# Kernel optimization log

Measured on AMD Instinct MI355X. Metric: run time of the kernel, lower is better.

Reference implementation:

```python
import jax, jax.numpy as jnp
import numpy as np

ALPHA = 5.0   # ATan surrogate sharpness
THETA = 1.0   # firing threshold
EPS = 1e-5    # BatchNorm eps

@jax.custom_vjp
def spike(x):
    # forward: heaviside; backward: ATan surrogate
    return (x >= 0.0).astype(x.dtype)

def _spike_fwd(x):
    return spike(x), x

def _spike_bwd(x, g):
    return (g * (ALPHA / 2.0) / (1.0 + (jnp.pi / 2.0 * ALPHA * x) ** 2),)

spike.defvjp(_spike_fwd, _spike_bwd)

def lif_layer(x, W, beta_p, gamma, bias, U0):
    # x: [B,T,J], W: [I,J] -> h: [B,T,I]
    h = jnp.einsum('btj,ij->bti', x, W)
    # BatchNorm1d in training mode: per-channel stats over B*T (biased var)
    mu = h.mean(axis=(0, 1))
    var = h.var(axis=(0, 1))
    h = (h - mu) * jax.lax.rsqrt(var + EPS) * gamma + bias
    beta = jax.nn.sigmoid(beta_p)  # [I]
    S0 = jnp.zeros_like(U0)

    def step(carry, xt):
        Ut, St = carry
        Ut = beta * (Ut - THETA * St) + (1.0 - beta) * xt  # soft reset
        St = spike(Ut - THETA)
        return (Ut, St), St

    _, o = jax.lax.scan(step, (U0, S0), jnp.swapaxes(h, 0, 1))  # [T,B,I]
    return jnp.swapaxes(o, 0, 1)  # [B,T,I]

def setup_inputs() -> dict:
    key = jax.random.key(0)
    B, T, J, H = 32, 1024, 1024, 2048
    ks = jax.random.split(key, 16)
    f32 = jnp.float32
    inp = {
        'x': jax.random.normal(ks[0], (B, T, J), f32),
        'W1': jax.random.normal(ks[1], (H, J), f32) / np.sqrt(J),
        'beta1': jax.random.uniform(ks[2], (H,), f32, 0.0, 4.0),
        'gamma1': jnp.ones((H,), f32),
        'bias1': jnp.zeros((H,), f32),
        'U01': jax.random.uniform(ks[3], (B, H), f32),
        'W2': jax.random.normal(ks[4], (H, H), f32) / np.sqrt(H),
        'beta2': jax.random.uniform(ks[5], (H,), f32, 0.0, 4.0),
        'gamma2': jnp.ones((H,), f32),
        'bias2': jnp.zeros((H,), f32),
        'U02': jax.random.uniform(ks[6], (B, H), f32),
        'W3': jax.random.normal(ks[7], (J, H), f32) / np.sqrt(H),
        'beta3': jax.random.uniform(ks[8], (J,), f32, 0.0, 4.0),
        'gamma3': jnp.ones((J,), f32),
        'bias3': jnp.zeros((J,), f32),
        'U03': jax.random.uniform(ks[9], (B, J), f32),
    }
    return inp

def reference(x, W1, beta1, gamma1, bias1, U01,
              W2, beta2, gamma2, bias2, U02,
              W3, beta3, gamma3, bias3, U03):
    h = lif_layer(x, W1, beta1, gamma1, bias1, U01)
    h = lif_layer(h, W2, beta2, gamma2, bias2, U02)
    h = lif_layer(h, W3, beta3, gamma3, bias3, U03)
    return h
```

## Files before the change

kernel.cpp:

```cpp
#include <hip/hip_runtime.h>
#include <hip/hip_bf16.h>
#include <cmath>

#define BB 32
#define TT 1024
#define JJ 1024
#define HH 2048
#define MM (BB * TT)
#define MHALF (MM / 2)

typedef short s8v __attribute__((ext_vector_type(8)));
typedef float f4v __attribute__((ext_vector_type(4)));
typedef unsigned int u4v __attribute__((ext_vector_type(4)));
union ABu { u4v u; s8v v; };

__device__ inline void split_bf16x3(float w, unsigned short& h,
                                    unsigned short& m, unsigned short& l) {
    __hip_bfloat16 bh = __float2bfloat16(w);
    const float fh = __bfloat162float(bh);
    const float r1 = w - fh;
    __hip_bfloat16 bm = __float2bfloat16(r1);
    const float fm = __bfloat162float(bm);
    __hip_bfloat16 bl = __float2bfloat16(r1 - fm);
    h = *(unsigned short*)&bh; m = *(unsigned short*)&bm; l = *(unsigned short*)&bl;
}

__global__ void split_w(const float* __restrict__ W,
                        unsigned short* __restrict__ ph,
                        unsigned short* __restrict__ pm,
                        unsigned short* __restrict__ pl, int n)
{
    const int i = blockIdx.x * 256 + threadIdx.x;
    if (i >= n) return;
    split_bf16x3(W[i], ph[i], pm[i], pl[i]);
}

__global__ __launch_bounds__(512) void mfma_spk_gemm(
    const unsigned char* __restrict__ S,
    const unsigned short* __restrict__ Wh,
    const unsigned short* __restrict__ Wm,
    const unsigned short* __restrict__ Wl,
    float* __restrict__ C, int M, int N, int K)
{
    __shared__ __align__(16) unsigned short Blds[2][3][2][128][32];
    const int tid = threadIdx.x;
    const int wv = tid >> 6;
    const int lane = tid & 63;
    const int wm = wv >> 1, wn = wv & 1;
    const int r16 = lane & 15, quad = lane >> 4;
    const int bm = blockIdx.x * 256;
    const int bn = blockIdx.y * 128;
    const int Kb = K >> 3;

    f4v acc[4][4] = {};

    const int rl = lane >> 2, chl = lane & 3;
    const int srow = wv * 16 + rl;
    const int kc = (chl - (srow >> 1)) & 3;
    const size_t soff = (size_t)(bn + srow) * K + kc * 8;
    const int ldsrow = wv * 16;

    size_t aoff[4];
#pragma unroll
    for (int ms = 0; ms < 4; ++ms)
        aoff[ms] = (size_t)(bm + wm * 64 + ms * 16 + r16) * Kb + quad;

    int bR[4], bC[4];
#pragma unroll
    for (int ns = 0; ns < 4; ++ns) {
        bR[ns] = wn * 64 + ns * 16 + r16;
        bC[ns] = ((quad + (bR[ns] >> 1)) & 3) * 8;
    }

    auto stage = [&](int buf, int p, int kh, int k0) {
        const unsigned short* Wp = (p == 0) ? Wh : (p == 1) ? Wm : Wl;
        __builtin_amdgcn_global_load_lds(
            (const __attribute__((address_space(1))) void*)(Wp + soff + k0 + kh * 32),
            (__attribute__((address_space(3))) void*)&Blds[buf][p][kh][ldsrow][0], 16, 0, 0);
    };

    unsigned int ab[2][4];
#pragma unroll
    for (int kh = 0; kh < 2; ++kh)
#pragma unroll
        for (int ms = 0; ms < 4; ++ms) ab[kh][ms] = S[aoff[ms] + kh * 4];

#pragma unroll
    for (int p = 0; p < 3; ++p)
#pragma unroll
        for (int kh = 0; kh < 2; ++kh) stage(0, p, kh, 0);

    const int NT = K >> 6;
    for (int t = 0; t < NT; ++t) {
        const int cur = t & 1, nxt = cur ^ 1;
        const int k0 = t << 6;
        __syncthreads();

        s8v afr[2][4];
#pragma unroll
        for (int kh = 0; kh < 2; ++kh)
#pragma unroll
            for (int ms = 0; ms < 4; ++ms) {
                ABu tu;
                const unsigned int b = ab[kh][ms];
                tu.u[0] = ((b        & 1u) * 0x3F80u) | (((b >> 1) & 1u) * 0x3F800000u);
                tu.u[1] = (((b >> 2) & 1u) * 0x3F80u) | (((b >> 3) & 1u) * 0x3F800000u);
                tu.u[2] = (((b >> 4) & 1u) * 0x3F80u) | (((b >> 5) & 1u) * 0x3F800000u);
                tu.u[3] = (((b >> 6) & 1u) * 0x3F80u) | (((b >> 7) & 1u) * 0x3F800000u);
                afr[kh][ms] = tu.v;
            }
        if (t + 1 < NT) {
            const size_t kb = (size_t)((k0 + 64) >> 3);
#pragma unroll
            for (int kh = 0; kh < 2; ++kh)
#pragma unroll
                for (int ms = 0; ms < 4; ++ms) ab[kh][ms] = S[aoff[ms] + kb + kh * 4];
        }

#pragma unroll
        for (int p = 0; p < 3; ++p)
#pragma unroll
            for (int kh = 0; kh < 2; ++kh) {
                s8v bf[4];
#pragma unroll
                for (int ns = 0; ns < 4; ++ns)
                    bf[ns] = *(const s8v*)&Blds[cur][p][kh][bR[ns]][bC[ns]];
                if (t + 1 < NT) stage(nxt, p, kh, k0 + 64);
                __builtin_amdgcn_s_setprio(1);
#pragma unroll
                for (int ms = 0; ms < 4; ++ms)
#pragma unroll
                    for (int ns = 0; ns < 4; ++ns)
                        acc[ms][ns] = __builtin_amdgcn_mfma_f32_16x16x32_bf16(
                            afr[kh][ms], bf[ns], acc[ms][ns], 0, 0, 0);
                __builtin_amdgcn_s_setprio(0);
            }
    }

#pragma unroll
    for (int ms = 0; ms < 4; ++ms)
#pragma unroll
        for (int ns = 0; ns < 4; ++ns) {
            const int row = bm + wm * 64 + ms * 16 + quad * 4;
            const int col = bn + wn * 64 + ns * 16 + r16;
#pragma unroll
            for (int r = 0; r < 4; ++r)
                C[(size_t)(row + r) * N + col] = acc[ms][ns][r];
        }
}

struct Sp3 { unsigned int o0, o1, o2; };

__device__ inline Sp3 split_pair(float x, float y)
{
    const unsigned int xb = __float_as_uint(x), yb = __float_as_uint(y);
    const unsigned int x0 = xb & 0xFFFF0000u,  y0 = yb & 0xFFFF0000u;
    const float xr1 = x - __uint_as_float(x0), yr1 = y - __uint_as_float(y0);
    const unsigned int x1b = __float_as_uint(xr1), y1b = __float_as_uint(yr1);
    const unsigned int x1 = x1b & 0xFFFF0000u, y1 = y1b & 0xFFFF0000u;
    const float xr2 = xr1 - __uint_as_float(x1), yr2 = yr1 - __uint_as_float(y1);
    Sp3 r;
    r.o0 = __builtin_amdgcn_perm(yb, xb, 0x07060302u);
    r.o1 = __builtin_amdgcn_perm(y1b, x1b, 0x07060302u);
    r.o2 = __builtin_amdgcn_perm(__float_as_uint(yr2), __float_as_uint(xr2), 0x07060302u);
    return r;
}

__global__ __launch_bounds__(256) void mfma_f32x3_gemm(
    const float* __restrict__ A,
    const unsigned short* __restrict__ Wh,
    const unsigned short* __restrict__ Wm,
    const unsigned short* __restrict__ Wl,
    float* __restrict__ C, int M, int N, int K)
{
    __shared__ __align__(16) unsigned short Blds[3][2][128][32];
    const int tid = threadIdx.x;
    const int wv = tid >> 6;
    const int lane = tid & 63;
    const int wm = wv >> 1, wn = wv & 1;
    const int r16 = lane & 15, quad = lane >> 4;

    const int lin = blockIdx.y * 16 + blockIdx.x;
    const int ppx = gridDim.y >> 3;
    const int xcd = lin & 7, li = lin >> 3;
    const int pm = xcd * ppx + (li >> 4);
    const int pn = li & 15;
    const int bm = pm * 128;
    const int bn = pn * 128;

    f4v acc[4][4] = {};

    const int rl = lane >> 2, chl = lane & 3;
    size_t soff[2];
    int ldsrow[2];
#pragma unroll
    for (int i = 0; i < 2; ++i) {
        const int r = wv * 32 + i * 16 + rl;
        const int kc = (chl - (r >> 1)) & 3;
        soff[i] = (size_t)(bn + r) * K + kc * 8;
        ldsrow[i] = wv * 32 + i * 16;
    }

    size_t aoff[4];
#pragma unroll
    for (int ms = 0; ms < 4; ++ms)
        aoff[ms] = (size_t)(bm + wm * 64 + ms * 16 + r16) * K + quad * 8;

    int bR[4], bC[4];
#pragma unroll
    for (int ns = 0; ns < 4; ++ns) {
        bR[ns] = wn * 64 + ns * 16 + r16;
        bC[ns] = ((quad + (bR[ns] >> 1)) & 3) * 8;
    }

    float4 av[2][4][2];
#pragma unroll
    for (int kh = 0; kh < 2; ++kh)
#pragma unroll
        for (int ms = 0; ms < 4; ++ms) {
            av[kh][ms][0] = *(const float4*)(A + aoff[ms] + kh * 32);
            av[kh][ms][1] = *(const float4*)(A + aoff[ms] + kh * 32 + 4);
        }

    for (int k0 = 0; k0 < K; k0 += 64) {
        __syncthreads();
#pragma unroll
        for (int i = 0; i < 2; ++i)
#pragma unroll
            for (int kh = 0; kh < 2; ++kh) {
                __builtin_amdgcn_global_load_lds(
                    (const __attribute__((address_space(1))) void*)(Wh + soff[i] + k0 + kh * 32),
                    (__attribute__((address_space(3))) void*)&Blds[0][kh][ldsrow[i]][0], 16, 0, 0);
                __builtin_amdgcn_global_load_lds(
                    (const __attribute__((address_space(1))) void*)(Wm + soff[i] + k0 + kh * 32),
                    (__attribute__((address_space(3))) void*)&Blds[1][kh][ldsrow[i]][0], 16, 0, 0);
                __builtin_amdgcn_global_load_lds(
                    (const __attribute__((address_space(1))) void*)(Wl + soff[i] + k0 + kh * 32),
                    (__attribute__((address_space(3))) void*)&Blds[2][kh][ldsrow[i]][0], 16, 0, 0);
            }
        s8v afr[3][2][4];
#pragma unroll
        for (int kh = 0; kh < 2; ++kh)
#pragma unroll
            for (int ms = 0; ms < 4; ++ms) {
                ABu t0, t1, t2;
                const float4 v0 = av[kh][ms][0];
                const float4 v1 = av[kh][ms][1];
                const Sp3 s0 = split_pair(v0.x, v0.y);
                const Sp3 s1 = split_pair(v0.z, v0.w);
                const Sp3 s2 = split_pair(v1.x, v1.y);
                const Sp3 s3 = split_pair(v1.z, v1.w);
                t0.u[0] = s0.o0; t1.u[0] = s0.o1; t2.u[0] = s0.o2;
                t0.u[1] = s1.o0; t1.u[1] = s1.o1; t2.u[1] = s1.o2;
                t0.u[2] = s2.o0; t1.u[2] = s2.o1; t2.u[2] = s2.o2;
                t0.u[3] = s3.o0; t1.u[3] = s3.o1; t2.u[3] = s3.o2;
                afr[0][kh][ms] = t0.v;
                afr[1][kh][ms] = t1.v;
                afr[2][kh][ms] = t2.v;
            }
        __syncthreads();
        if (k0 + 64 < K) {
#pragma unroll
            for (int kh = 0; kh < 2; ++kh)
#pragma unroll
                for (int ms = 0; ms < 4; ++ms) {
                    av[kh][ms][0] = *(const float4*)(A + aoff[ms] + k0 + 64 + kh * 32);
                    av[kh][ms][1] = *(const float4*)(A + aoff[ms] + k0 + 64 + kh * 32 + 4);
                }
        }
#pragma unroll
        for (int kh = 0; kh < 2; ++kh)
#pragma unroll
            for (int pw = 0; pw < 3; ++pw) {
                s8v bf[4];
#pragma unroll
                for (int ns = 0; ns < 4; ++ns)
                    bf[ns] = *(const s8v*)&Blds[pw][kh][bR[ns]][bC[ns]];
#pragma unroll
                for (int pa = 0; pa + pw < 3; ++pa)
#pragma unroll
                    for (int ms = 0; ms < 4; ++ms)
#pragma unroll
                        for (int ns = 0; ns < 4; ++ns)
                            acc[ms][ns] = __builtin_amdgcn_mfma_f32_16x16x32_bf16(
                                afr[pa][kh][ms], bf[ns], acc[ms][ns], 0, 0, 0);
            }
    }

#pragma unroll
    for (int ms = 0; ms < 4; ++ms)
#pragma unroll
        for (int ns = 0; ns < 4; ++ns) {
            const int row = bm + wm * 64 + ms * 16 + quad * 4;
            const int col = bn + wn * 64 + ns * 16 + r16;
#pragma unroll
            for (int r = 0; r < 4; ++r)
                C[(size_t)(row + r) * N + col] = acc[ms][ns][r];
        }
}

#define RCHUNK 128

__global__ void bn_stats_partial2(const float* __restrict__ hA,
                                  const float* __restrict__ hB,
                                  float* __restrict__ partial, int N)
{
    const int n = blockIdx.x * 256 + threadIdx.x;
    const int chunk = blockIdx.y;
    const int half = (MM / RCHUNK) / 2;
    const float* __restrict__ h = (chunk < half) ? hA : hB;
    const int cl = chunk & (half - 1);
    const float* p = h + (size_t)cl * RCHUNK * N + n;
    float s = 0.f, s2 = 0.f;
#pragma unroll 4
    for (int r = 0; r < RCHUNK; ++r) {
        const float v = p[(size_t)r * N];
        s += v;
        s2 = fmaf(v, v, s2);
    }
    partial[((size_t)chunk * 2 + 0) * N + n] = s;
    partial[((size_t)chunk * 2 + 1) * N + n] = s2;
}

__global__ void bn_stats_final(const float* __restrict__ partial,
                               float* __restrict__ stats,
                               int N, int nchunks)
{
    const int n = blockIdx.x * 256 + threadIdx.x;
    double s = 0.0, s2 = 0.0;
    for (int c = 0; c < nchunks; ++c) {
        s  += (double)partial[((size_t)c * 2 + 0) * N + n];
        s2 += (double)partial[((size_t)c * 2 + 1) * N + n];
    }
    const double inv_m = 1.0 / (double)MM;
    const double mu = s * inv_m;
    const double var = s2 * inv_m - mu * mu;
    stats[n]     = (float)mu;
    stats[N + n] = (float)(1.0 / sqrt(var + 1e-5));
}

#define LIF_STEP_PACK(hv)                                            \
    do {                                                             \
        const float hn = ((hv) - mu) * rstd * g + bi;                \
        u = beta * (u - s) + omb * hn;                               \
        const bool sp = (u - 1.0f) >= 0.f;                           \
        s = sp ? 1.f : 0.f;                                          \
        const unsigned long long mball = __ballot(sp);               \
        if (lead) bits[widx] = mball;                                \
        widx += nw;                                                  \
    } while (0)

#define LIF_LOAD8(buf, tbase)                                        \
    _Pragma("unroll")                                                \
    for (int j = 0; j < 8; ++j) {                                    \
        const int tl = (tbase) + j;                                  \
        buf[j] = h[base + (size_t)(tl < TT ? tl : TT - 1) * N];      \
    }

__global__ __launch_bounds__(64) void bn_lif_scan_pack2(
    const float* __restrict__ hA,
    const float* __restrict__ hB,
    unsigned long long* __restrict__ bits,
    const float* __restrict__ stats,
    const float* __restrict__ gamma,
    const float* __restrict__ bias,
    const float* __restrict__ beta_p,
    const float* __restrict__ U0,
    int N)
{
    const int n = blockIdx.x * 64 + threadIdx.x;
    const int b = blockIdx.y;
    const float* __restrict__ h = (b < BB / 2) ? hA : hB;
    const int bl = b & (BB / 2 - 1);
    const int nw = N >> 6;
    const float mu = stats[n];
    const float rstd = stats[N + n];
    const float g = gamma[n];
    const float bi = bias[n];
    const float beta = 1.f / (1.f + expf(-beta_p[n]));
    const float omb = 1.f - beta;
    float u = U0[(size_t)b * N + n];
    float s = 0.f;
    const size_t base = ((size_t)bl * TT) * N + n;
    size_t widx = ((size_t)b * TT) * nw + (n >> 6);
    const bool lead = (threadIdx.x & 63) == 0;

    float b0[8], b1[8], b2[8], b3[8];
    LIF_LOAD8(b0, 0);
    LIF_LOAD8(b1, 8);
    LIF_LOAD8(b2, 16);
    for (int t0 = 0; t0 < TT; t0 += 32) {
        LIF_LOAD8(b3, t0 + 24);
#pragma unroll
        for (int j = 0; j < 8; ++j) { const float hv = b0[j]; LIF_STEP_PACK(hv); }
        LIF_LOAD8(b0, t0 + 32);
#pragma unroll
        for (int j = 0; j < 8; ++j) { const float hv = b1[j]; LIF_STEP_PACK(hv); }
        LIF_LOAD8(b1, t0 + 40);
#pragma unroll
        for (int j = 0; j < 8; ++j) { const float hv = b2[j]; LIF_STEP_PACK(hv); }
        LIF_LOAD8(b2, t0 + 48);
#pragma unroll
        for (int j = 0; j < 8; ++j) { const float hv = b3[j]; LIF_STEP_PACK(hv); }
    }
}

#define LIF_STEP_F32(hv)                                             \
    do {                                                             \
        const float hn = ((hv) - mu) * rstd * g + bi;                \
        u = beta * (u - s) + omb * hn;                               \
        s = ((u - 1.0f) >= 0.f) ? 1.f : 0.f;                         \
        out[oidx] = s;                                               \
        oidx += N;                                                   \
    } while (0)

__global__ __launch_bounds__(64) void bn_lif_scan_f32_2(
    const float* __restrict__ h,
    float* __restrict__ out,
    const float* __restrict__ stats,
    const float* __restrict__ gamma,
    const float* __restrict__ bias,
    const float* __restrict__ beta_p,
    const float* __restrict__ U0,
    int N)
{
    const int n = blockIdx.x * 64 + threadIdx.x;
    const int b = blockIdx.y;
    const float mu = stats[n];
    const float rstd = stats[N + n];
    const float g = gamma[n];
    const float bi = bias[n];
    const float beta = 1.f / (1.f + expf(-beta_p[n]));
    const float omb = 1.f - beta;
    float u = U0[(size_t)b * N + n];
    float s = 0.f;
    const size_t base = ((size_t)b * TT) * N + n;
    size_t oidx = base;

    float b0[8], b1[8], b2[8], b3[8];
    LIF_LOAD8(b0, 0);
    LIF_LOAD8(b1, 8);
    LIF_LOAD8(b2, 16);
    for (int t0 = 0; t0 < TT; t0 += 32) {
        LIF_LOAD8(b3, t0 + 24);
#pragma unroll
        for (int j = 0; j < 8; ++j) { const float hv = b0[j]; LIF_STEP_F32(hv); }
        LIF_LOAD8(b0, t0 + 32);
#pragma unroll
        for (int j = 0; j < 8; ++j) { const float hv = b1[j]; LIF_STEP_F32(hv); }
        LIF_LOAD8(b1, t0 + 40);
#pragma unroll
        for (int j = 0; j < 8; ++j) { const float hv = b2[j]; LIF_STEP_F32(hv); }
        LIF_LOAD8(b2, t0 + 48);
#pragma unroll
        for (int j = 0; j < 8; ++j) { const float hv = b3[j]; LIF_STEP_F32(hv); }
    }
}

extern "C" void kernel_launch(void* const* d_in, const int* in_sizes, int n_in,
                              void* d_out, int out_size, void* d_ws, size_t ws_size,
                              hipStream_t stream)
{
    const float* x   = (const float*)d_in[0];
    const float* W1  = (const float*)d_in[1];
    const float* bp1 = (const float*)d_in[2];
    const float* g1  = (const float*)d_in[3];
    const float* bi1 = (const float*)d_in[4];
    const float* U01 = (const float*)d_in[5];
    const float* W2  = (const float*)d_in[6];
    const float* bp2 = (const float*)d_in[7];
    const float* g2  = (const float*)d_in[8];
    const float* bi2 = (const float*)d_in[9];
    const float* U02 = (const float*)d_in[10];
    const float* W3  = (const float*)d_in[11];
    const float* bp3 = (const float*)d_in[12];
    const float* g3  = (const float*)d_in[13];
    const float* bi3 = (const float*)d_in[14];
    const float* U03 = (const float*)d_in[15];
    float* out = (float*)d_out;

    unsigned char* ws = (unsigned char*)d_ws;
    const size_t HA_BYTES  = (size_t)MHALF * HH * sizeof(float);
    const size_t SPK_BYTES = (size_t)MM * (HH / 8);
    float*              hA   = (float*)ws;
    float*              hB   = (float*)d_out;
    unsigned long long* spk  = (unsigned long long*)(ws + HA_BYTES);
    float*              part = (float*)(ws + HA_BYTES + SPK_BYTES);
    float*              stat = (float*)(ws + HA_BYTES + SPK_BYTES + 4194304);
    unsigned short*     W2h  = (unsigned short*)(ws + HA_BYTES + SPK_BYTES + 4194304 + 16384);
    unsigned short*     W2m  = W2h + (size_t)HH * HH;
    unsigned short*     W2l  = W2m + (size_t)HH * HH;
    unsigned short*     W3h  = W2l + (size_t)HH * HH;
    unsigned short*     W3m  = W3h + (size_t)JJ * HH;
    unsigned short*     W3l  = W3m + (size_t)JJ * HH;

    const dim3 blk(256);
    const dim3 blk64(64);
    const dim3 blk512(512);
    const int nck = MM / RCHUNK;

    split_w<<<dim3((HH * JJ) / 256), blk, 0, stream>>>(W1, W2h, W2m, W2l, HH * JJ);
    mfma_f32x3_gemm<<<dim3(HH / 128, MHALF / 128), blk, 0, stream>>>(
        x, W2h, W2m, W2l, hA, MHALF, HH, JJ);
    mfma_f32x3_gemm<<<dim3(HH / 128, MHALF / 128), blk, 0, stream>>>(
        x + (size_t)MHALF * JJ, W2h, W2m, W2l, hB, MHALF, HH, JJ);
    split_w<<<dim3((HH * HH) / 256), blk, 0, stream>>>(W2, W2h, W2m, W2l, HH * HH);
    split_w<<<dim3((JJ * HH) / 256), blk, 0, stream>>>(W3, W3h, W3m, W3l, JJ * HH);

    bn_stats_partial2<<<dim3(HH / 256, nck), blk, 0, stream>>>(hA, hB, part, HH);
    bn_stats_final<<<dim3(HH / 256), blk, 0, stream>>>(part, stat, HH, nck);
    bn_lif_scan_pack2<<<dim3(HH / 64, BB), blk64, 0, stream>>>(
        hA, hB, spk, stat, g1, bi1, bp1, U01, HH);

    mfma_spk_gemm<<<dim3(MHALF / 256, HH / 128), blk512, 0, stream>>>(
        (const unsigned char*)spk, W2h, W2m, W2l, hA, MHALF, HH, HH);
    mfma_spk_gemm<<<dim3(MHALF / 256, HH / 128), blk512, 0, stream>>>(
        (const unsigned char*)spk + (size_t)MHALF * (HH / 8), W2h, W2m, W2l, hB, MHALF, HH, HH);
    bn_stats_partial2<<<dim3(HH / 256, nck), blk, 0, stream>>>(hA, hB, part, HH);
    bn_stats_final<<<dim3(HH / 256), blk, 0, stream>>>(part, stat, HH, nck);
    bn_lif_scan_pack2<<<dim3(HH / 64, BB), blk64, 0, stream>>>(
        hA, hB, spk, stat, g2, bi2, bp2, U02, HH);

    mfma_spk_gemm<<<dim3(MM / 256, JJ / 128), blk512, 0, stream>>>(
        (const unsigned char*)spk, W3h, W3m, W3l, hA, MM, JJ, HH);
    bn_stats_partial2<<<dim3(JJ / 256, nck), blk, 0, stream>>>(
        hA, hA + (size_t)MHALF * JJ, part, JJ);
    bn_stats_final<<<dim3(JJ / 256), blk, 0, stream>>>(part, stat, JJ, nck);
    bn_lif_scan_f32_2<<<dim3(JJ / 64, BB), blk64, 0, stream>>>(
        hA, out, stat, g3, bi3, bp3, U03, JJ);
}
```

Before: 2.703 ms.

## Double-buffer B tiles in LDS and prefetch next stage before compute

The f32x3 GEMM now uses two LDS buffers with a K-step of 32, issuing the global-to-LDS loads for the next tile at the start of each iteration. This lets those loads overlap with the MFMA work on the current tile and removes one of the two barriers per iteration. The spike-input GEMM also moves its next-tile staging to the top of the loop and keeps a single trailing barrier. The trade-off is twice as many loop iterations, each doing less work, so fixed per-iteration overhead grows.

```diff
diff --git a/kernel.cpp b/kernel.cpp
--- a/kernel.cpp
+++ b/kernel.cpp
@@ -89,12 +89,19 @@
     for (int p = 0; p < 3; ++p)
 #pragma unroll
         for (int kh = 0; kh < 2; ++kh) stage(0, p, kh, 0);
+    __syncthreads();
 
     const int NT = K >> 6;
     for (int t = 0; t < NT; ++t) {
         const int cur = t & 1, nxt = cur ^ 1;
         const int k0 = t << 6;
-        __syncthreads();
+
+        if (t + 1 < NT) {
+#pragma unroll
+            for (int p = 0; p < 3; ++p)
+#pragma unroll
+                for (int kh = 0; kh < 2; ++kh) stage(nxt, p, kh, k0 + 64);
+        }
 
         s8v afr[2][4];
 #pragma unroll
@@ -125,7 +132,6 @@
 #pragma unroll
                 for (int ns = 0; ns < 4; ++ns)
                     bf[ns] = *(const s8v*)&Blds[cur][p][kh][bR[ns]][bC[ns]];
-                if (t + 1 < NT) stage(nxt, p, kh, k0 + 64);
                 __builtin_amdgcn_s_setprio(1);
 #pragma unroll
                 for (int ms = 0; ms < 4; ++ms)
@@ -135,6 +141,8 @@
                             afr[kh][ms], bf[ns], acc[ms][ns], 0, 0, 0);
                 __builtin_amdgcn_s_setprio(0);
             }
+
+        if (t + 1 < NT) __syncthreads();
     }
 
 #pragma unroll
@@ -173,7 +181,7 @@
     const unsigned short* __restrict__ Wl,
     float* __restrict__ C, int M, int N, int K)
 {
-    __shared__ __align__(16) unsigned short Blds[3][2][128][32];
+    __shared__ __align__(16) unsigned short Blds[2][3][128][32];
     const int tid = threadIdx.x;
     const int wv = tid >> 6;
     const int lane = tid & 63;
@@ -195,10 +203,10 @@
     int ldsrow[2];
 #pragma unroll
     for (int i = 0; i < 2; ++i) {
-        const int r = wv * 32 + i * 16 + rl;
+        const int r = i * 64 + wv * 16 + rl;
         const int kc = (chl - (r >> 1)) & 3;
         soff[i] = (size_t)(bn + r) * K + kc * 8;
-        ldsrow[i] = wv * 32 + i * 16;
+        ldsrow[i] = i * 64 + wv * 16;
     }
 
     size_t aoff[4];
@@ -213,78 +221,82 @@
         bC[ns] = ((quad + (bR[ns] >> 1)) & 3) * 8;
     }
 
-    float4 av[2][4][2];
-#pragma unroll
-    for (int kh = 0; kh < 2; ++kh)
+    auto stage = [&](int buf, int p, int i, int k0) {
+        const unsigned short* Wp = (p == 0) ? Wh : (p == 1) ? Wm : Wl;
+        __builtin_amdgcn_global_load_lds(
+            (const __attribute__((address_space(1))) void*)(Wp + soff[i] + k0),
+            (__attribute__((address_space(3))) void*)&Blds[buf][p][ldsrow[i]][0], 16, 0, 0);
+    };
+
+    float4 av[4][2];
+#pragma unroll
+    for (int ms = 0; ms < 4; ++ms) {
+        av[ms][0] = *(const float4*)(A + aoff[ms]);
+        av[ms][1] = *(const float4*)(A + aoff[ms] + 4);
+    }
+#pragma unroll
+    for (int p = 0; p < 3; ++p)
+#pragma unroll
+        for (int i = 0; i < 2; ++i) stage(0, p, i, 0);
+    __syncthreads();
+
+    const int NT = K >> 5;
+    for (int t = 0; t < NT; ++t) {
+        const int cur = t & 1, nxt = cur ^ 1;
+        const int k0 = t << 5;
+
+        if (t + 1 < NT) {
+#pragma unroll
+            for (int p = 0; p < 3; ++p)
+#pragma unroll
+                for (int i = 0; i < 2; ++i) stage(nxt, p, i, k0 + 32);
+        }
+
+        s8v afr[3][4];
 #pragma unroll
         for (int ms = 0; ms < 4; ++ms) {
-            av[kh][ms][0] = *(const float4*)(A + aoff[ms] + kh * 32);
-            av[kh][ms][1] = *(const float4*)(A + aoff[ms] + kh * 32 + 4);
-        }
-
-    for (int k0 = 0; k0 < K; k0 += 64) {
-        __syncthreads();
-#pragma unroll
-        for (int i = 0; i < 2; ++i)
-#pragma unroll
-            for (int kh = 0; kh < 2; ++kh) {
-                __builtin_amdgcn_global_load_lds(
-                    (const __attribute__((address_space(1))) void*)(Wh + soff[i] + k0 + kh * 32),
-                    (__attribute__((address_space(3))) void*)&Blds[0][kh][ldsrow[i]][0], 16, 0, 0);
-                __builtin_amdgcn_global_load_lds(
-                    (const __attribute__((address_space(1))) void*)(Wm + soff[i] + k0 + kh * 32),
-                    (__attribute__((address_space(3))) void*)&Blds[1][kh][ldsrow[i]][0], 16, 0, 0);
-                __builtin_amdgcn_global_load_lds(
-                    (const __attribute__((address_space(1))) void*)(Wl + soff[i] + k0 + kh * 32),
-                    (__attribute__((address_space(3))) void*)&Blds[2][kh][ldsrow[i]][0], 16, 0, 0);
+            ABu t0, t1, t2;
+            const float4 v0 = av[ms][0];
+            const float4 v1 = av[ms][1];
+            const Sp3 s0 = split_pair(v0.x, v0.y);
+            const Sp3 s1 = split_pair(v0.z, v0.w);
+            const Sp3 s2 = split_pair(v1.x, v1.y);
+            const Sp3 s3 = split_pair(v1.z, v1.w);
+            t0.u[0] = s0.o0; t1.u[0] = s0.o1; t2.u[0] = s0.o2;
+            t0.u[1] = s1.o0; t1.u[1] = s1.o1; t2.u[1] = s1.o2;
+            t0.u[2] = s2.o0; t1.u[2] = s2.o1; t2.u[2] = s2.o2;
+            t0.u[3] = s3.o0; t1.u[3] = s3.o1; t2.u[3] = s3.o2;
+            afr[0][ms] = t0.v;
+            afr[1][ms] = t1.v;
+            afr[2][ms] = t2.v;
+        }
+        if (t + 1 < NT) {
+#pragma unroll
+            for (int ms = 0; ms < 4; ++ms) {
+                av[ms][0] = *(const float4*)(A + aoff[ms] + k0 + 32);
+                av[ms][1] = *(const float4*)(A + aoff[ms] + k0 + 32 + 4);
             }
-        s8v afr[3][2][4];
-#pragma unroll
-        for (int kh = 0; kh < 2; ++kh)
-#pragma unroll
-            for (int ms = 0; ms < 4; ++ms) {
-                ABu t0, t1, t2;
-                const float4 v0 = av[kh][ms][0];
-                const float4 v1 = av[kh][ms][1];
-                const Sp3 s0 = split_pair(v0.x, v0.y);
-                const Sp3 s1 = split_pair(v0.z, v0.w);
-                const Sp3 s2 = split_pair(v1.x, v1.y);
-                const Sp3 s3 = split_pair(v1.z, v1.w);
-                t0.u[0] = s0.o0; t1.u[0] = s0.o1; t2.u[0] = s0.o2;
-                t0.u[1] = s1.o0; t1.u[1] = s1.o1; t2.u[1] = s1.o2;
-                t0.u[2] = s2.o0; t1.u[2] = s2.o1; t2.u[2] = s2.o2;
-                t0.u[3] = s3.o0; t1.u[3] = s3.o1; t2.u[3] = s3.o2;
-                afr[0][kh][ms] = t0.v;
-                afr[1][kh][ms] = t1.v;
-                afr[2][kh][ms] = t2.v;
-            }
-        __syncthreads();
-        if (k0 + 64 < K) {
-#pragma unroll
-            for (int kh = 0; kh < 2; ++kh)
-#pragma unroll
-                for (int ms = 0; ms < 4; ++ms) {
-                    av[kh][ms][0] = *(const float4*)(A + aoff[ms] + k0 + 64 + kh * 32);
-                    av[kh][ms][1] = *(const float4*)(A + aoff[ms] + k0 + 64 + kh * 32 + 4);
-                }
-        }
-#pragma unroll
-        for (int kh = 0; kh < 2; ++kh)
-#pragma unroll
-            for (int pw = 0; pw < 3; ++pw) {
-                s8v bf[4];
-#pragma unroll
-                for (int ns = 0; ns < 4; ++ns)
-                    bf[ns] = *(const s8v*)&Blds[pw][kh][bR[ns]][bC[ns]];
-#pragma unroll
-                for (int pa = 0; pa + pw < 3; ++pa)
-#pragma unroll
-                    for (int ms = 0; ms < 4; ++ms)
-#pragma unroll
-                        for (int ns = 0; ns < 4; ++ns)
-                            acc[ms][ns] = __builtin_amdgcn_mfma_f32_16x16x32_bf16(
-                                afr[pa][kh][ms], bf[ns], acc[ms][ns], 0, 0, 0);
-            }
+        }
+
+#pragma unroll
+        for (int pw = 0; pw < 3; ++pw) {
+            s8v bf[4];
+#pragma unroll
+            for (int ns = 0; ns < 4; ++ns)
+                bf[ns] = *(const s8v*)&Blds[cur][pw][bR[ns]][bC[ns]];
+            __builtin_amdgcn_s_setprio(1);
+#pragma unroll
+            for (int pa = 0; pa + pw < 3; ++pa)
+#pragma unroll
+                for (int ms = 0; ms < 4; ++ms)
+#pragma unroll
+                    for (int ns = 0; ns < 4; ++ns)
+                        acc[ms][ns] = __builtin_amdgcn_mfma_f32_16x16x32_bf16(
+                            afr[pa][ms], bf[ns], acc[ms][ns], 0, 0, 0);
+            __builtin_amdgcn_s_setprio(0);
+        }
+
+        if (t + 1 < NT) __syncthreads();
     }
 
 #pragma unroll
```

Result: faster. 2.499 ms (-7.5%).
